# Optimization experiments

Hardware: AMD Instinct MI355X
Metric: run time of the kernel (lower is better)

Reference implementation:

```python
import jax, jax.numpy as jnp
import numpy as np

GAMMA = 0.999   # from TDLoss.__init__ default
LAMBDA = 0.95   # from compute_gae default lambda_
B, S = 8192, 2048


def setup_inputs() -> dict:
    key = jax.random.key(0)
    k1, k2, k3, k4 = jax.random.split(key, 4)
    rewards = jax.random.normal(k1, (B, S), dtype=jnp.float32)
    values = jax.random.normal(k2, (B, S), dtype=jnp.float32)
    dones = jax.random.randint(k3, (B, S), 0, 2).astype(jnp.int32)
    # prefix validity mask: valid_len[b] = mask[b].sum(), as assumed by compute_gae
    lengths = jax.random.randint(k4, (B,), S // 2, S + 1)
    mask = (jnp.arange(S)[None, :] < lengths[:, None]).astype(jnp.int32)
    return {"rewards": rewards, "values": values, "dones": dones, "mask": mask}


def _gae(rewards, values, dones_f, mask, gamma, lam):
    # rewards/values/dones_f: [B,S] float; mask: [B,S] int prefix mask
    b, s = rewards.shape
    valid_len = mask.sum(axis=1)                      # [B]
    t_idx = jnp.arange(s)
    valid = t_idx[None, :] < valid_len[:, None]       # [B,S] bool
    is_last = t_idx[None, :] == (valid_len[:, None] - 1)
    # next_value = values[:, t+1], except 0 at the last valid step (and at t=S-1)
    next_vals = jnp.concatenate([values[:, 1:], jnp.zeros((b, 1), values.dtype)], axis=1)
    next_vals = jnp.where(is_last, jnp.zeros((), values.dtype), next_vals)
    nd = 1.0 - dones_f                                # (1 - done)
    delta = rewards + gamma * next_vals * nd - values

    def step(gae, xs):
        d_t, nd_t, valid_t = xs                        # each [B]
        g = d_t + gamma * lam * nd_t * gae
        g = jnp.where(valid_t, g, jnp.zeros((), d_t.dtype))  # zero outside valid prefix; resets carry
        return g, g

    xs = (delta.T, nd.T, valid.T)                     # time-major [S,B]
    _, adv_t = jax.lax.scan(step, jnp.zeros(b, rewards.dtype), xs, reverse=True)
    advantages = adv_t.T                              # [B,S]
    returns = jnp.where(valid, advantages + values, jnp.zeros((), values.dtype))
    return advantages, returns


def reference(rewards, values, dones, mask):
    return _gae(rewards, values, dones.astype(jnp.float32), mask, GAMMA, LAMBDA)
```

## Files before the change

kernel.cpp:

```cpp
#include <hip/hip_runtime.h>


static constexpr int BATCH = 8192;
static constexpr int SEQ   = 2048;
static constexpr float GAMMA      = 0.999f;
static constexpr float LAMBDA     = 0.95f;
static constexpr float GL         = GAMMA * LAMBDA;
static constexpr float INV_LAMBDA = 1.0f / LAMBDA;

__global__ __launch_bounds__(256, 4) void gae_kernel(
    const float* __restrict__ rewards,
    const float* __restrict__ values,
    const int*   __restrict__ dones,
    const int*   __restrict__ mask,
    float*       __restrict__ out)
{
    const int tid  = threadIdx.x;
    const int lane = tid & 63;
    const int w    = tid >> 6;
    const size_t rowbase = (size_t)blockIdx.x * SEQ;
    const int    t0  = tid << 3;
    const size_t off = rowbase + (size_t)t0;

    __shared__ int   s_len;
    __shared__ float s_Aw[4];
    __shared__ float s_Bw[4];

    float4 r0, r1, v0, v1;
    int4   d0, d1;
    float  vnext = 0.0f;

    const bool early = (w < 2);
    if (early) {
        r0 = *reinterpret_cast<const float4*>(rewards + off);
        r1 = *reinterpret_cast<const float4*>(rewards + off + 4);
        v0 = *reinterpret_cast<const float4*>(values  + off);
        v1 = *reinterpret_cast<const float4*>(values  + off + 4);
        d0 = *reinterpret_cast<const int4*>(dones + off);
        d1 = *reinterpret_cast<const int4*>(dones + off + 4);
        if (lane == 63) vnext = values[off + 8];
    }

    if (w == 0) {
        int msamp = 0;
        if (lane < 16)
            msamp = mask[rowbase + 1024u + ((unsigned)lane << 6)];
        const int k    = __popcll(__ballot(msamp != 0));
        const int base = 960 + (k << 6);
        const int mf   = mask[rowbase + (unsigned)(base + lane)];
        const int len  = base + __popcll(__ballot(mf != 0));
        if (lane == 0) s_len = len;
    }
    __syncthreads();

    const int len    = s_len;
    const int nvalid = len - t0;

    if (!early) {
        if (nvalid > 0) {
            r0 = *reinterpret_cast<const float4*>(rewards + off);
            r1 = *reinterpret_cast<const float4*>(rewards + off + 4);
            v0 = *reinterpret_cast<const float4*>(values  + off);
            v1 = *reinterpret_cast<const float4*>(values  + off + 4);
            d0 = *reinterpret_cast<const int4*>(dones + off);
            d1 = *reinterpret_cast<const int4*>(dones + off + 4);
            if (lane == 63 && (t0 + 8 < len)) vnext = values[off + 8];
        } else {
            r0 = r1 = v0 = v1 = make_float4(0.f, 0.f, 0.f, 0.f);
            d0 = d1 = make_int4(0, 0, 0, 0);
        }
    }

    const float rr[8] = {r0.x, r0.y, r0.z, r0.w, r1.x, r1.y, r1.z, r1.w};
    const float vv[8] = {v0.x, v0.y, v0.z, v0.w, v1.x, v1.y, v1.z, v1.w};
    const int   dd[8] = {d0.x, d0.y, d0.z, d0.w, d1.x, d1.y, d1.z, d1.w};

    float a[8], b[8], vm[8];
    #pragma unroll
    for (int e = 0; e < 8; ++e) {
        const bool m  = (e < nvalid);
        const bool mn = m && (dd[e] == 0);
        vm[e] = m ? vv[e] : 0.0f;
        a[e]  = mn ? GL : 0.0f;
        b[e]  = (m ? rr[e] : 0.0f) - vm[e];
    }

    float nv7 = __shfl_down(vm[0], 1, 64);
    if (lane == 63) nv7 = (t0 + 8 < len) ? vnext : 0.0f;

    #pragma unroll
    for (int e = 0; e < 8; ++e) {
        const float nv = (e < 7) ? vm[e + 1] : nv7;
        b[e] = fmaf(a[e] * INV_LAMBDA, nv, b[e]);
    }

    float A = a[7], B = b[7];
    #pragma unroll
    for (int e = 6; e >= 0; --e) {
        B = fmaf(a[e], B, b[e]);
        A *= a[e];
    }

    float As = A, Bs = B;
    #pragma unroll
    for (int d = 1; d < 64; d <<= 1) {
        const float Ao = __shfl_down(As, d, 64);
        const float Bo = __shfl_down(Bs, d, 64);
        if (lane + d < 64) {
            Bs = fmaf(As, Bo, Bs);
            As *= Ao;
        }
    }

    if (lane == 0) { s_Aw[w] = As; s_Bw[w] = Bs; }
    __syncthreads();

    float C = 0.0f;
    for (int u = 3; u > w; --u)
        C = fmaf(s_Aw[u], C, s_Bw[u]);

    float cA = __shfl_down(As, 1, 64);
    float cB = __shfl_down(Bs, 1, 64);
    if (lane == 63) { cA = 1.0f; cB = 0.0f; }
    float g = fmaf(cA, C, cB);

    float adv[8], ret[8];
    #pragma unroll
    for (int e = 7; e >= 0; --e) {
        g = fmaf(a[e], g, b[e]);
        adv[e] = g;
        ret[e] = g + vm[e];
    }

    *reinterpret_cast<float4*>(out + off) =
        make_float4(adv[0], adv[1], adv[2], adv[3]);
    *reinterpret_cast<float4*>(out + off + 4) =
        make_float4(adv[4], adv[5], adv[6], adv[7]);
    const size_t roff = (size_t)BATCH * SEQ + off;
    *reinterpret_cast<float4*>(out + roff) =
        make_float4(ret[0], ret[1], ret[2], ret[3]);
    *reinterpret_cast<float4*>(out + roff + 4) =
        make_float4(ret[4], ret[5], ret[6], ret[7]);
}

extern "C" void kernel_launch(void* const* d_in, const int* in_sizes, int n_in,
                              void* d_out, int out_size, void* d_ws, size_t ws_size,
                              hipStream_t stream) {
    const float* rewards = (const float*)d_in[0];
    const float* values  = (const float*)d_in[1];
    const int*   dones   = (const int*)d_in[2];
    const int*   mask    = (const int*)d_in[3];
    float* out = (float*)d_out;

    dim3 grid(BATCH), block(256);
    gae_kernel<<<grid, block, 0, stream>>>(rewards, values, dones, mask, out);
}
```

Baseline: 302.8 us.

## Precompute row lengths in a separate kernel and use nontemporal output stores

Moves the per-row valid-length search out of the main GAE kernel into a small prepass kernel that writes the lengths to workspace. The main kernel then reads one int per row instead of doing ballot-based mask probing followed by a block-wide barrier, so all waves can start their loads without waiting. Output stores become nontemporal to reduce cache pollution on the write stream. This adds a second kernel launch and a dependent global read, and falls back to the old path when the workspace is too small.

```diff
diff --git a/kernel.cpp b/kernel.cpp
--- a/kernel.cpp
+++ b/kernel.cpp
@@ -8,11 +8,31 @@
 static constexpr float GL         = GAMMA * LAMBDA;
 static constexpr float INV_LAMBDA = 1.0f / LAMBDA;
 
+typedef float f32x4 __attribute__((ext_vector_type(4)));
+
+__global__ __launch_bounds__(256, 8) void len_kernel(
+    const int* __restrict__ mask, int* __restrict__ lens)
+{
+    const int lane = threadIdx.x & 63;
+    const int row  = (blockIdx.x << 2) + (threadIdx.x >> 6);
+    const size_t rowbase = (size_t)row * SEQ;
+
+    int ms = 0;
+    if (lane < 16) ms = mask[rowbase + 1024u + ((unsigned)lane << 6)];
+    const int k    = __popcll(__ballot(ms != 0));
+    const int base = 960 + (k << 6);
+    const int mf   = mask[rowbase + (unsigned)(base + lane)];
+    const int len  = base + __popcll(__ballot(mf != 0));
+    if (lane == 0) lens[row] = len;
+}
+
+template<bool USE_LENS>
 __global__ __launch_bounds__(256, 4) void gae_kernel(
     const float* __restrict__ rewards,
     const float* __restrict__ values,
     const int*   __restrict__ dones,
     const int*   __restrict__ mask,
+    const int*   __restrict__ lens,
     float*       __restrict__ out)
 {
     const int tid  = threadIdx.x;
@@ -22,9 +42,9 @@
     const int    t0  = tid << 3;
     const size_t off = rowbase + (size_t)t0;
 
-    __shared__ int   s_len;
     __shared__ float s_Aw[4];
     __shared__ float s_Bw[4];
+    __shared__ int   s_len;
 
     float4 r0, r1, v0, v1;
     int4   d0, d1;
@@ -41,19 +61,24 @@
         if (lane == 63) vnext = values[off + 8];
     }
 
-    if (w == 0) {
-        int msamp = 0;
-        if (lane < 16)
-            msamp = mask[rowbase + 1024u + ((unsigned)lane << 6)];
-        const int k    = __popcll(__ballot(msamp != 0));
-        const int base = 960 + (k << 6);
-        const int mf   = mask[rowbase + (unsigned)(base + lane)];
-        const int len  = base + __popcll(__ballot(mf != 0));
-        if (lane == 0) s_len = len;
+    int len;
+    if constexpr (USE_LENS) {
+        len = lens[blockIdx.x];
+    } else {
+        if (w == 0) {
+            int ms = 0;
+            if (lane < 16)
+                ms = mask[rowbase + 1024u + ((unsigned)lane << 6)];
+            const int k    = __popcll(__ballot(ms != 0));
+            const int base = 960 + (k << 6);
+            const int mf   = mask[rowbase + (unsigned)(base + lane)];
+            const int l    = base + __popcll(__ballot(mf != 0));
+            if (lane == 0) s_len = l;
+        }
+        __syncthreads();
+        len = s_len;
     }
-    __syncthreads();
 
-    const int len    = s_len;
     const int nvalid = len - t0;
 
     if (!early) {
@@ -132,15 +157,15 @@
         ret[e] = g + vm[e];
     }
 
-    *reinterpret_cast<float4*>(out + off) =
-        make_float4(adv[0], adv[1], adv[2], adv[3]);
-    *reinterpret_cast<float4*>(out + off + 4) =
-        make_float4(adv[4], adv[5], adv[6], adv[7]);
+    const f32x4 a0 = {adv[0], adv[1], adv[2], adv[3]};
+    const f32x4 a1 = {adv[4], adv[5], adv[6], adv[7]};
+    const f32x4 t0v = {ret[0], ret[1], ret[2], ret[3]};
+    const f32x4 t1v = {ret[4], ret[5], ret[6], ret[7]};
+    __builtin_nontemporal_store(a0, reinterpret_cast<f32x4*>(out + off));
+    __builtin_nontemporal_store(a1, reinterpret_cast<f32x4*>(out + off + 4));
     const size_t roff = (size_t)BATCH * SEQ + off;
-    *reinterpret_cast<float4*>(out + roff) =
-        make_float4(ret[0], ret[1], ret[2], ret[3]);
-    *reinterpret_cast<float4*>(out + roff + 4) =
-        make_float4(ret[4], ret[5], ret[6], ret[7]);
+    __builtin_nontemporal_store(t0v, reinterpret_cast<f32x4*>(out + roff));
+    __builtin_nontemporal_store(t1v, reinterpret_cast<f32x4*>(out + roff + 4));
 }
 
 extern "C" void kernel_launch(void* const* d_in, const int* in_sizes, int n_in,
@@ -152,6 +177,13 @@
     const int*   mask    = (const int*)d_in[3];
     float* out = (float*)d_out;
 
-    dim3 grid(BATCH), block(256);
-    gae_kernel<<<grid, block, 0, stream>>>(rewards, values, dones, mask, out);
+    if (ws_size >= (size_t)BATCH * sizeof(int)) {
+        int* lens = (int*)d_ws;
+        len_kernel<<<dim3(BATCH / 4), dim3(256), 0, stream>>>(mask, lens);
+        gae_kernel<true><<<dim3(BATCH), dim3(256), 0, stream>>>(
+            rewards, values, dones, mask, lens, out);
+    } else {
+        gae_kernel<false><<<dim3(BATCH), dim3(256), 0, stream>>>(
+            rewards, values, dones, mask, nullptr, out);
+    }
 }
```

After: 316.7 us. 4.6% more time.
